# Performance work log

Measured on AMD Instinct MI355X. Metric: run time of the kernel, lower is better.

## Reference

```python
import jax, jax.numpy as jnp
import numpy as np

H, KB = 8, 8          # z_num grid (h, k)
OB, IB = 64, 64       # per-call weight block [OB, IB, K]
K, L = 9, 9           # kernel dims of exe_unet_weight and unet_1d_weights
ZD, PD, DH = 64, 16, 128  # z_dim, pde_inputs dim, hypernet hidden


def setup_inputs() -> dict:
    key = jax.random.key(0)
    k1, k2, k3, k4, k5 = jax.random.split(key, 5)
    # z params: torch.fmod(randn, 2) as in the original __init__
    z_all = jnp.fmod(jax.random.normal(k1, (H * KB, ZD), jnp.float32), 2.0)
    W1 = jax.random.normal(k2, (DH, ZD + PD), jnp.float32) * 0.1
    b1 = jnp.zeros((DH,), jnp.float32)
    W2 = jax.random.normal(k3, (OB * IB * K, DH), jnp.float32) * 0.02
    b2 = jnp.zeros((OB * IB * K,), jnp.float32)
    unet_1d_weights = jax.random.normal(k4, (H * OB, KB * IB, L), jnp.float32)
    pde_inputs = jax.random.normal(k5, (PD,), jnp.float32)
    return {"z_all": z_all, "W1": W1, "b1": b1, "W2": W2, "b2": b2,
            "unet_1d_weights": unet_1d_weights, "pde_inputs": pde_inputs}


def reference(z_all, W1, b1, W2, b2, unet_1d_weights, pde_inputs):
    # Batched hypernet: one GEMM over all h*k z vectors instead of h*k calls.
    x = jnp.concatenate([z_all, jnp.broadcast_to(pde_inputs, (H * KB, PD))], axis=1)  # [hk, ZD+PD]
    hid = jax.nn.relu(x @ W1.T + b1)                    # [hk, DH]
    w = (hid @ W2.T + b2).reshape(H, KB, OB, IB, K)      # per-cell blocks
    # cat(dim=1) within row, cat(dim=0) across rows -> [H*OB, KB*IB, K]
    exe_unet_weight = w.transpose(0, 2, 1, 3, 4).reshape(H * OB, KB * IB, K)
    # broadcast outer product over kernel dims
    w_2d = jnp.einsum('oik,oil->oikl', exe_unet_weight, unet_1d_weights)
    return w_2d
```

## Files before the change

kernel.cpp:

```cpp
#include <hip/hip_runtime.h>

#define ZD_ 64
#define PD_ 16
#define DH_ 128

__global__ void hid_kernel(const float* __restrict__ z_all,
                           const float* __restrict__ W1,
                           const float* __restrict__ b1,
                           const float* __restrict__ pde,
                           float* __restrict__ hidT) {
    int gid = blockIdx.x * 256 + threadIdx.x;
    int d = gid >> 6;
    int r = gid & 63;
    const float* w = W1 + d * (ZD_ + PD_);
    const float* z = z_all + r * ZD_;
    float acc = b1[d];
    #pragma unroll 8
    for (int c = 0; c < ZD_; ++c) acc += z[c] * w[c];
    #pragma unroll
    for (int c = 0; c < PD_; ++c) acc += pde[c] * w[ZD_ + c];
    hidT[d * 64 + r] = fmaxf(acc, 0.0f);
}

#define SMEM_FLOATS 13456

__global__ __launch_bounds__(256) void fused_kernel(
        const float* __restrict__ hidT,
        const float* __restrict__ W2,
        const float* __restrict__ b2,
        const float* __restrict__ unet,
        float* __restrict__ out) {
    __shared__ __align__(16) float smem[SMEM_FLOATS];
    float* s_w2 = smem;
    float* s_hT = smem + 4752;

    int tid = threadIdx.x;
    int b   = blockIdx.x;
    int ob  = b >> 4;
    int ibp = b & 15;
    int n0  = ob * 576 + ibp * 36;

    const float4* g4 = reinterpret_cast<const float4*>(W2 + (size_t)n0 * DH_);
    #pragma unroll
    for (int t = 0; t < 5; ++t) {
        int j = t * 256 + tid;
        if (j < 1152) {
            int row = j >> 5;
            int c4  = j & 31;
            *reinterpret_cast<float4*>(&s_w2[row * 132 + c4 * 4]) = g4[j];
        }
    }
    const float4* h4g = reinterpret_cast<const float4*>(hidT);
    #pragma unroll
    for (int t = 0; t < 8; ++t) {
        int j  = t * 256 + tid;
        int d  = j >> 4;
        int r4 = j & 15;
        *reinterpret_cast<float4*>(&s_hT[d * 68 + r4 * 4]) = h4g[j];
    }

    int cp  = tid & 31;
    int ibl = (tid >> 5) & 3;
    int ks  = tid >> 7;

    float2 acc[9];
    if (ks == 0) {
        #pragma unroll
        for (int kk = 0; kk < 9; ++kk) {
            float bv = b2[n0 + ibl * 9 + kk];
            acc[kk] = make_float2(bv, bv);
        }
    } else {
        #pragma unroll
        for (int kk = 0; kk < 9; ++kk) acc[kk] = make_float2(0.f, 0.f);
    }
    __syncthreads();

    const float* wbase = s_w2 + ibl * 9 * 132 + ks * 64;
    const float* hbase = s_hT + ks * 64 * 68 + 2 * cp;
    #pragma unroll 4
    for (int cc = 0; cc < 64; cc += 4) {
        float2 h0 = *reinterpret_cast<const float2*>(&hbase[(cc + 0) * 68]);
        float2 h1 = *reinterpret_cast<const float2*>(&hbase[(cc + 1) * 68]);
        float2 h2 = *reinterpret_cast<const float2*>(&hbase[(cc + 2) * 68]);
        float2 h3 = *reinterpret_cast<const float2*>(&hbase[(cc + 3) * 68]);
        #pragma unroll
        for (int kk = 0; kk < 9; ++kk) {
            float4 w = *reinterpret_cast<const float4*>(&wbase[kk * 132 + cc]);
            acc[kk].x += h0.x * w.x + h1.x * w.y + h2.x * w.z + h3.x * w.w;
            acc[kk].y += h0.y * w.x + h1.y * w.y + h2.y * w.z + h3.y * w.w;
        }
    }
    __syncthreads();

    float* s_exe = smem;
    float* s_red = smem + 2368;
    float* s_un  = smem + 4816;

    if (ks == 1) {
        int slot = tid & 127;
        #pragma unroll
        for (int kk = 0; kk < 9; ++kk) {
            s_red[slot * 19 + kk]     = acc[kk].x;
            s_red[slot * 19 + 9 + kk] = acc[kk].y;
        }
    }
    for (int j = tid; j < 576; j += 256) {
        int cell = j / 9;
        int q    = j - cell * 9;
        int hh = cell >> 3, kb = cell & 7;
        size_t gb = ((size_t)((hh * 64 + ob) * 512 + kb * 64 + ibp * 4)) * 9;
        *reinterpret_cast<float4*>(&s_un[cell * 36 + q * 4]) =
            *reinterpret_cast<const float4*>(unet + gb + q * 4);
    }
    __syncthreads();

    if (ks == 0) {
        #pragma unroll
        for (int kk = 0; kk < 9; ++kk) {
            int col = ibl * 9 + kk;
            s_exe[(2 * cp + 0) * 37 + col] = acc[kk].x + s_red[tid * 19 + kk];
            s_exe[(2 * cp + 1) * 37 + col] = acc[kk].y + s_red[tid * 19 + 9 + kk];
        }
    }
    __syncthreads();

    for (int idx = tid; idx < 5184; idx += 256) {
        int cell = idx / 81;
        int q    = idx - cell * 81;
        float4 v;
        float* vp = &v.x;
        #pragma unroll
        for (int j2 = 0; j2 < 4; ++j2) {
            int e    = q * 4 + j2;
            int ibl2 = e / 81;
            int rem  = e - ibl2 * 81;
            int k    = rem / 9;
            int l    = rem - k * 9;
            vp[j2] = s_exe[cell * 37 + ibl2 * 9 + k]
                   * s_un [cell * 36 + ibl2 * 9 + l];
        }
        int hh = cell >> 3, kb = cell & 7;
        size_t gb = ((size_t)((hh * 64 + ob) * 512 + kb * 64 + ibp * 4)) * 81;
        reinterpret_cast<float4*>(out + gb)[q] = v;
    }
}

extern "C" void kernel_launch(void* const* d_in, const int* in_sizes, int n_in,
                              void* d_out, int out_size, void* d_ws, size_t ws_size,
                              hipStream_t stream) {
    const float* z_all = (const float*)d_in[0];
    const float* W1    = (const float*)d_in[1];
    const float* b1    = (const float*)d_in[2];
    const float* W2    = (const float*)d_in[3];
    const float* b2    = (const float*)d_in[4];
    const float* unet  = (const float*)d_in[5];
    const float* pde   = (const float*)d_in[6];
    float* out = (float*)d_out;

    float* hidT = (float*)d_ws;

    hid_kernel<<<32, 256, 0, stream>>>(z_all, W1, b1, pde, hidT);
    fused_kernel<<<1024, 256, 0, stream>>>(hidT, W2, b2, unet, out);
}
```

Baseline: 148.8 us.

## Split hypernet GEMM reduction over four waves with 4x9 register tiles

Remaps the per-block W2·hid GEMM so each wave handles a 32-wide slice of the hidden dimension and each thread computes a 4-column by 9-row register tile instead of 2 by 9. The partial sums of the four waves are combined through shared memory. Shared-memory padding is removed, and launch bounds now request 3 blocks per SM for higher occupancy. The larger tile raises FMA work per shared-memory load, but removing the padding may cause LDS bank conflicts, and the reduction now costs more shared-memory traffic.

New measurement: 144.2 us. 3.1% less time.

```diff
diff --git a/kernel.cpp b/kernel.cpp
--- a/kernel.cpp
+++ b/kernel.cpp
@@ -22,9 +22,9 @@
     hidT[d * 64 + r] = fmaxf(acc, 0.0f);
 }
 
-#define SMEM_FLOATS 13456
+#define SMEM_FLOATS 12800
 
-__global__ __launch_bounds__(256) void fused_kernel(
+__global__ __launch_bounds__(256, 3) void fused_kernel(
         const float* __restrict__ hidT,
         const float* __restrict__ W2,
         const float* __restrict__ b2,
@@ -32,13 +32,22 @@
         float* __restrict__ out) {
     __shared__ __align__(16) float smem[SMEM_FLOATS];
     float* s_w2 = smem;
-    float* s_hT = smem + 4752;
+    float* s_hT = smem + 4608;
 
     int tid = threadIdx.x;
     int b   = blockIdx.x;
     int ob  = b >> 4;
     int ibp = b & 15;
     int n0  = ob * 576 + ibp * 36;
+
+    int lane = tid & 63;
+    int wave = tid >> 6;
+    int cg   = lane & 15;
+    int ibl  = lane >> 4;
+
+    float b2v[9];
+    #pragma unroll
+    for (int kk = 0; kk < 9; ++kk) b2v[kk] = b2[n0 + ibl * 9 + kk];
 
     const float4* g4 = reinterpret_cast<const float4*>(W2 + (size_t)n0 * DH_);
     #pragma unroll
@@ -47,7 +56,7 @@
         if (j < 1152) {
             int row = j >> 5;
             int c4  = j & 31;
-            *reinterpret_cast<float4*>(&s_w2[row * 132 + c4 * 4]) = g4[j];
+            *reinterpret_cast<float4*>(&s_w2[row * 128 + c4 * 4]) = g4[j];
         }
     }
     const float4* h4g = reinterpret_cast<const float4*>(hidT);
@@ -56,53 +65,46 @@
         int j  = t * 256 + tid;
         int d  = j >> 4;
         int r4 = j & 15;
-        *reinterpret_cast<float4*>(&s_hT[d * 68 + r4 * 4]) = h4g[j];
-    }
-
-    int cp  = tid & 31;
-    int ibl = (tid >> 5) & 3;
-    int ks  = tid >> 7;
-
-    float2 acc[9];
-    if (ks == 0) {
-        #pragma unroll
-        for (int kk = 0; kk < 9; ++kk) {
-            float bv = b2[n0 + ibl * 9 + kk];
-            acc[kk] = make_float2(bv, bv);
-        }
-    } else {
-        #pragma unroll
-        for (int kk = 0; kk < 9; ++kk) acc[kk] = make_float2(0.f, 0.f);
+        *reinterpret_cast<float4*>(&s_hT[d * 64 + r4 * 4]) = h4g[j];
     }
     __syncthreads();
 
-    const float* wbase = s_w2 + ibl * 9 * 132 + ks * 64;
-    const float* hbase = s_hT + ks * 64 * 68 + 2 * cp;
-    #pragma unroll 4
-    for (int cc = 0; cc < 64; cc += 4) {
-        float2 h0 = *reinterpret_cast<const float2*>(&hbase[(cc + 0) * 68]);
-        float2 h1 = *reinterpret_cast<const float2*>(&hbase[(cc + 1) * 68]);
-        float2 h2 = *reinterpret_cast<const float2*>(&hbase[(cc + 2) * 68]);
-        float2 h3 = *reinterpret_cast<const float2*>(&hbase[(cc + 3) * 68]);
+    const float* wb = s_w2 + wave * 32;
+    const float* hb = s_hT + wave * 32 * 64 + 4 * cg;
+    float4 acc[9];
+    #pragma unroll
+    for (int kk = 0; kk < 9; ++kk) acc[kk] = make_float4(0.f, 0.f, 0.f, 0.f);
+
+    #pragma unroll 2
+    for (int cc = 0; cc < 32; cc += 4) {
+        float4 h0 = *reinterpret_cast<const float4*>(&hb[(cc + 0) * 64]);
+        float4 h1 = *reinterpret_cast<const float4*>(&hb[(cc + 1) * 64]);
+        float4 h2 = *reinterpret_cast<const float4*>(&hb[(cc + 2) * 64]);
+        float4 h3 = *reinterpret_cast<const float4*>(&hb[(cc + 3) * 64]);
         #pragma unroll
         for (int kk = 0; kk < 9; ++kk) {
-            float4 w = *reinterpret_cast<const float4*>(&wbase[kk * 132 + cc]);
+            float4 w = *reinterpret_cast<const float4*>(
+                           &wb[(ibl * 9 + kk) * 128 + cc]);
             acc[kk].x += h0.x * w.x + h1.x * w.y + h2.x * w.z + h3.x * w.w;
             acc[kk].y += h0.y * w.x + h1.y * w.y + h2.y * w.z + h3.y * w.w;
+            acc[kk].z += h0.z * w.x + h1.z * w.y + h2.z * w.z + h3.z * w.w;
+            acc[kk].w += h0.w * w.x + h1.w * w.y + h2.w * w.z + h3.w * w.w;
         }
     }
     __syncthreads();
 
-    float* s_exe = smem;
-    float* s_red = smem + 2368;
-    float* s_un  = smem + 4816;
+    float* s_red = smem;
+    float* s_exe = smem + 7104;
+    float* s_un  = smem + 9472;
 
-    if (ks == 1) {
-        int slot = tid & 127;
+    if (wave != 0) {
+        int base = ((wave - 1) * 64 + lane) * 37;
         #pragma unroll
         for (int kk = 0; kk < 9; ++kk) {
-            s_red[slot * 19 + kk]     = acc[kk].x;
-            s_red[slot * 19 + 9 + kk] = acc[kk].y;
+            s_red[base +      kk] = acc[kk].x;
+            s_red[base +  9 + kk] = acc[kk].y;
+            s_red[base + 18 + kk] = acc[kk].z;
+            s_red[base + 27 + kk] = acc[kk].w;
         }
     }
     for (int j = tid; j < 576; j += 256) {
@@ -115,12 +117,27 @@
     }
     __syncthreads();
 
-    if (ks == 0) {
+    if (wave == 0) {
         #pragma unroll
         for (int kk = 0; kk < 9; ++kk) {
-            int col = ibl * 9 + kk;
-            s_exe[(2 * cp + 0) * 37 + col] = acc[kk].x + s_red[tid * 19 + kk];
-            s_exe[(2 * cp + 1) * 37 + col] = acc[kk].y + s_red[tid * 19 + 9 + kk];
+            float bv = b2v[kk];
+            int col  = ibl * 9 + kk;
+            float rx = acc[kk].x + s_red[(      lane) * 37 +      kk]
+                                 + s_red[( 64 + lane) * 37 +      kk]
+                                 + s_red[(128 + lane) * 37 +      kk];
+            float ry = acc[kk].y + s_red[(      lane) * 37 +  9 + kk]
+                                 + s_red[( 64 + lane) * 37 +  9 + kk]
+                                 + s_red[(128 + lane) * 37 +  9 + kk];
+            float rz = acc[kk].z + s_red[(      lane) * 37 + 18 + kk]
+                                 + s_red[( 64 + lane) * 37 + 18 + kk]
+                                 + s_red[(128 + lane) * 37 + 18 + kk];
+            float rw = acc[kk].w + s_red[(      lane) * 37 + 27 + kk]
+                                 + s_red[( 64 + lane) * 37 + 27 + kk]
+                                 + s_red[(128 + lane) * 37 + 27 + kk];
+            s_exe[(4 * cg + 0) * 37 + col] = rx + bv;
+            s_exe[(4 * cg + 1) * 37 + col] = ry + bv;
+            s_exe[(4 * cg + 2) * 37 + col] = rz + bv;
+            s_exe[(4 * cg + 3) * 37 + col] = rw + bv;
         }
     }
     __syncthreads();
```
